# Optimization experiments

Measured on AMD Instinct MI355X. Metric: run time of the kernel, lower is better.

## Reference

```python
import jax, jax.numpy as jnp
import numpy as np

D_MODEL = 1024
N_HEADS = 16
HEAD_DIM = 64
BATCH = 4
SEQ = 2048


def setup_inputs() -> dict:
    key = jax.random.key(0)
    ks = jax.random.split(key, 5)
    scale = 1.0 / np.sqrt(D_MODEL)
    return {
        "x": jax.random.normal(ks[0], (BATCH, SEQ, D_MODEL), dtype=jnp.float32),
        "Wq": jax.random.normal(ks[1], (D_MODEL, N_HEADS * HEAD_DIM), dtype=jnp.float32) * scale,
        "Wk": jax.random.normal(ks[2], (D_MODEL, N_HEADS * HEAD_DIM), dtype=jnp.float32) * scale,
        "Wv": jax.random.normal(ks[3], (D_MODEL, N_HEADS * HEAD_DIM), dtype=jnp.float32) * scale,
        "Wo": jax.random.normal(ks[4], (N_HEADS * HEAD_DIM, D_MODEL), dtype=jnp.float32) * scale,
        "bo": jnp.zeros((D_MODEL,), dtype=jnp.float32),
    }


def reference(x, Wq, Wk, Wv, Wo, bo):
    B, S, _ = x.shape
    H, Dh = N_HEADS, HEAD_DIM
    # projections -> [B, H, S, Dh]
    q = (x @ Wq).reshape(B, S, H, Dh).transpose(0, 2, 1, 3)
    k = (x @ Wk).reshape(B, S, H, Dh).transpose(0, 2, 1, 3)
    v = (x @ Wv).reshape(B, S, H, Dh).transpose(0, 2, 1, 3)
    score = jnp.einsum("bhsd,bhtd->bhst", q, k) / jnp.sqrt(jnp.float32(Dh))
    causal = jnp.triu(jnp.ones((S, S), dtype=bool), k=1)
    score = jnp.where(causal, -jnp.inf, score)
    attn_probs = jax.nn.softmax(score, axis=-1)
    # dropout is identity in eval mode
    attn = jnp.einsum("bhst,bhtd->bhsd", attn_probs, v)
    out = attn.transpose(0, 2, 1, 3).reshape(B, S, H * Dh)
    out = out @ Wo + bo
    return (out, attn_probs)
```

## Files before the change

kernel.cpp:

```cpp
#include <hip/hip_runtime.h>
#include <hip/hip_bf16.h>

typedef __attribute__((ext_vector_type(8))) short bf16x8;
typedef __attribute__((ext_vector_type(4))) float f32x4;
typedef unsigned short ushort_t;
typedef unsigned int uint_t;

#define AS1 __attribute__((address_space(1)))
#define AS3 __attribute__((address_space(3)))

__constant__ int P4tab[16] = {0, 5, 10, 15, 1, 4, 11, 14, 2, 7, 8, 13, 3, 6, 9, 12};

__device__ __forceinline__ void gload_lds16(const void* g, void* l) {
    __builtin_amdgcn_global_load_lds((const AS1 void*)g, (AS3 void*)l, 16, 0, 0);
}

__device__ __forceinline__ ushort_t f2b(float f) {
    unsigned u = __builtin_bit_cast(unsigned, f);
    unsigned r = (u + 0x7FFFu + ((u >> 16) & 1u)) >> 16;
    return (ushort_t)r;
}

__global__ __launch_bounds__(256) void convert_x_kernel(const float* __restrict__ in,
                                                        ushort_t* __restrict__ out, int n4) {
    int i = blockIdx.x * blockDim.x + threadIdx.x;
    if (i < n4) {
        float4 f = ((const float4*)in)[i];
        ushort4 u;
        u.x = f2b(f.x); u.y = f2b(f.y); u.z = f2b(f.z); u.w = f2b(f.w);
        ((ushort4*)out)[i] = u;
    }
}

__global__ __launch_bounds__(256) void transpose_w_kernel(const float* __restrict__ W,
                                                          ushort_t* __restrict__ WT) {
    __shared__ float t[32][33];
    int n0 = blockIdx.x * 32, k0 = blockIdx.y * 32;
    int tx = threadIdx.x, ty = threadIdx.y;
    for (int i = 0; i < 4; ++i)
        t[ty + i * 8][tx] = W[(size_t)(k0 + ty + i * 8) * 1024 + n0 + tx];
    __syncthreads();
    for (int i = 0; i < 4; ++i)
        WT[(size_t)(n0 + ty + i * 8) * 1024 + k0 + tx] = f2b(t[tx][ty + i * 8]);
}

template <int N, int OUT_BF16>
__global__ __launch_bounds__(256) void gemm_kernel(const ushort_t* __restrict__ A,
                                                   const ushort_t* __restrict__ BT,
                                                   ushort_t* __restrict__ Cb,
                                                   float* __restrict__ Cf,
                                                   const float* __restrict__ bias) {
    const int K = 1024;
    __shared__ ushort_t As[3 * 128 * 32];
    __shared__ ushort_t Bs[3 * 128 * 32];
    int tid = threadIdx.x;
    int wid = tid >> 6, lane = tid & 63;
    int g = lane >> 4, lr = lane & 15;

    int zz = (int)blockIdx.x + 64 * (int)blockIdx.y;
    int nwg = 64 * (int)gridDim.y;
    int zs = (zz & 7) * (nwg >> 3) + (zz >> 3);
    int m0 = (zs % 64) * 128, n0 = (zs / 64) * 128;

    int wm = wid >> 1, wn = wid & 1;

    f32x4 acc[4][4] = {};

    int c0 = wid * 2;
    int lrow = lane >> 2;
    int lcol = ((lane & 3) ^ ((lane >> 3) & 3)) * 8;
    const ushort_t* Ag0 = A  + (size_t)(m0 + c0 * 16 + lrow) * K + lcol;
    const ushort_t* Ag1 = A  + (size_t)(m0 + c0 * 16 + 16 + lrow) * K + lcol;
    const ushort_t* Bg0 = BT + (size_t)(n0 + c0 * 16 + lrow) * K + lcol;
    const ushort_t* Bg1 = BT + (size_t)(n0 + c0 * 16 + 16 + lrow) * K + lcol;

    int swzA = ((lr >> 1) & 3) << 4;

    auto stage = [&](int si, int kt) {
        char* a0 = (char*)As + si * 8192 + c0 * 1024;
        char* b0 = (char*)Bs + si * 8192 + c0 * 1024;
        gload_lds16(Ag0 + kt * 32, a0);
        gload_lds16(Ag1 + kt * 32, a0 + 1024);
        gload_lds16(Bg0 + kt * 32, b0);
        gload_lds16(Bg1 + kt * 32, b0 + 1024);
    };

    stage(0, 0);
    stage(1, 1);
    asm volatile("s_waitcnt vmcnt(4)" ::: "memory");
    __builtin_amdgcn_s_barrier();
    __builtin_amdgcn_sched_barrier(0);
    for (int kt = 0; kt < 32; ++kt) {
        int nt = kt + 2;
        stage(nt % 3, nt < 32 ? nt : 31);
        const char* ab = (const char*)As + (kt % 3) * 8192;
        const char* bb = (const char*)Bs + (kt % 3) * 8192;
        bf16x8 af[4], bfr[4];
#pragma unroll
        for (int m = 0; m < 4; ++m) {
            int row = wm * 64 + m * 16 + lr;
            af[m] = *(const bf16x8*)(ab + row * 64 + ((g * 16) ^ swzA));
        }
#pragma unroll
        for (int n = 0; n < 4; ++n) {
            int row = wn * 64 + n * 16 + lr;
            bfr[n] = *(const bf16x8*)(bb + row * 64 + ((g * 16) ^ swzA));
        }
#pragma unroll
        for (int m = 0; m < 4; ++m)
#pragma unroll
            for (int n = 0; n < 4; ++n)
                acc[m][n] = __builtin_amdgcn_mfma_f32_16x16x32_bf16(af[m], bfr[n], acc[m][n], 0, 0, 0);
        asm volatile("s_waitcnt vmcnt(4)" ::: "memory");
        __builtin_amdgcn_s_barrier();
        __builtin_amdgcn_sched_barrier(0);
    }

#pragma unroll
    for (int m = 0; m < 4; ++m)
#pragma unroll
        for (int n = 0; n < 4; ++n) {
            int row0 = m0 + wm * 64 + m * 16 + g * 4;
            int col  = n0 + wn * 64 + n * 16 + lr;
#pragma unroll
            for (int r = 0; r < 4; ++r) {
                float v = acc[m][n][r];
                if (OUT_BF16)
                    Cb[(size_t)(row0 + r) * N + col] = f2b(v);
                else
                    Cf[(size_t)(row0 + r) * N + col] = v + bias[col];
            }
        }
}

__global__ __launch_bounds__(256) void vt_kernel(const ushort_t* __restrict__ Cqkv,
                                                 ushort_t* __restrict__ Vt) {
    int b = blockIdx.z, h = blockIdx.y, st = blockIdx.x;
    __shared__ ushort_t t[64][72];
    const ushort_t* src = Cqkv + (size_t)b * 2048 * 3072 + 2048 + (size_t)h * 64;
    int tid = threadIdx.x;
#pragma unroll
    for (int i = 0; i < 2; ++i) {
        int c = tid + i * 256;
        int sl = c >> 3, dc = (c & 7) * 8;
        *(bf16x8*)&t[sl][dc] = *(const bf16x8*)(src + (size_t)(st * 64 + sl) * 3072 + dc);
    }
    __syncthreads();
#pragma unroll
    for (int i = 0; i < 2; ++i) {
        int c = tid + i * 256;
        int d = c >> 3, sc = (c & 7) * 8;
        bf16x8 v;
#pragma unroll
        for (int j = 0; j < 8; ++j) v[j] = (short)t[sc + j][d];
        *(bf16x8*)(Vt + ((size_t)(b * 16 + h) * 64 + d) * 2048 + st * 64 + sc) = v;
    }
}

__global__ __launch_bounds__(256, 4) void attn_kernel(const ushort_t* __restrict__ Cqkv,
                                                      const ushort_t* __restrict__ Vtg,
                                                      float* __restrict__ Pout,
                                                      ushort_t* __restrict__ Oout) {
    const int S = 2048, DQ = 3072;
    const float C1 = 0.18033688f;
    const float C2 = 5.77078016f;

    int z = (int)blockIdx.x;
    int c = z & 255, j = z >> 8;
    int p = P4tab[(c & 3) * 4 + j];
    int h = (c >> 2) & 15, b = c >> 6;
    int qtA = p, qtB = 31 - p;

    int tid = threadIdx.x, wid = tid >> 6, lane = tid & 63;
    int g = lane >> 4, lr = lane & 15;
    int vsr = tid >> 2, vsc = (tid & 3) * 16;

    __shared__ ushort_t KV[4][4096];
    __shared__ ushort_t Pl[4096];
    char* PlB = (char*)Pl + wid * 2048;

    const ushort_t* Qb = Cqkv + (size_t)b * S * DQ + (size_t)h * 64;
    const ushort_t* Kb = Cqkv + (size_t)b * S * DQ + 1024 + (size_t)h * 64;
    const ushort_t* Vb = Vtg + (size_t)((b * 16 + h) * 64) * 2048;
    float* PbaseA = Pout + (((size_t)(b * 16 + h)) * S + qtA * 64) * S;
    float* PbaseB = Pout + (((size_t)(b * 16 + h)) * S + qtB * 64) * S;

    int srow = lane >> 3;
    int scol = ((lane & 7) ^ srow) * 8;

    auto zfill = [&](int zi) {
        float* base; int tt;
        if (zi < 31 - qtA) { base = PbaseA; tt = qtA + 1 + zi; }
        else               { base = PbaseB; tt = qtB + 1 + (zi - (31 - qtA)); }
        float* dst = base + (size_t)vsr * S + tt * 64 + vsc;
        f32x4 zf = {0.f, 0.f, 0.f, 0.f};
#pragma unroll
        for (int jj = 0; jj < 4; ++jj) ((f32x4*)dst)[jj] = zf;
    };

    auto stageK = [&](int ri, int tt) {
        char* dst = (char*)&KV[ri][0] + wid * 1024;
        gload_lds16(Kb + (size_t)(tt * 64 + wid * 8 + srow) * DQ + scol, dst);
        gload_lds16(Kb + (size_t)(tt * 64 + 32 + wid * 8 + srow) * DQ + scol, dst + 4096);
    };
    auto stageV = [&](int ri, int tt) {
        char* dst = (char*)&KV[2 + ri][0] + wid * 1024;
        gload_lds16(Vb + (size_t)(wid * 8 + srow) * 2048 + tt * 64 + scol, dst);
        gload_lds16(Vb + (size_t)(32 + wid * 8 + srow) * 2048 + tt * 64 + scol, dst + 4096);
    };
    auto stageK2 = [&](int ss, int t0, int t1) {
        char* dst = (char*)&KV[ss * 2][0] + wid * 1024;
        gload_lds16(Kb + (size_t)(t0 * 64 + wid * 8 + srow) * DQ + scol, dst);
        gload_lds16(Kb + (size_t)(t0 * 64 + 32 + wid * 8 + srow) * DQ + scol, dst + 4096);
        gload_lds16(Kb + (size_t)(t1 * 64 + wid * 8 + srow) * DQ + scol, dst + 8192);
        gload_lds16(Kb + (size_t)(t1 * 64 + 32 + wid * 8 + srow) * DQ + scol, dst + 12288);
    };

    bf16x8 qfA[2], qfB[2];
    {
        const ushort_t* qa = Qb + (size_t)(qtA * 64 + wid * 16 + lr) * DQ + g * 8;
        qfA[0] = *(const bf16x8*)qa;
        qfA[1] = *(const bf16x8*)(qa + 32);
        const ushort_t* qb2 = Qb + (size_t)(qtB * 64 + wid * 16 + lr) * DQ + g * 8;
        qfB[0] = *(const bf16x8*)qb2;
        qfB[1] = *(const bf16x8*)(qb2 + 32);
    }
    int qloc = wid * 16 + lr;

    float psA = 0.f, psB = 0.f;

    auto p1_tile = [&](const char* ksb, int tt) {
#pragma unroll
        for (int nb = 0; nb < 4; ++nb) {
            int row = nb * 16 + lr;
            int x = (row & 7) << 4;
            bf16x8 k0 = *(const bf16x8*)(ksb + row * 128 + ((g * 16) ^ x));
            bf16x8 k1 = *(const bf16x8*)(ksb + row * 128 + ((64 + g * 16) ^ x));
            f32x4 sB = {};
            sB = __builtin_amdgcn_mfma_f32_16x16x32_bf16(k0, qfB[0], sB, 0, 0, 0);
            sB = __builtin_amdgcn_mfma_f32_16x16x32_bf16(k1, qfB[1], sB, 0, 0, 0);
            if (tt == qtB) {
#pragma unroll
                for (int r = 0; r < 4; ++r)
                    if (nb * 16 + g * 4 + r <= qloc) psB += exp2f(fmaf(sB[r], C1, -C2));
            } else {
#pragma unroll
                for (int r = 0; r < 4; ++r) psB += exp2f(fmaf(sB[r], C1, -C2));
            }
            if (tt <= qtA) {
                f32x4 sA = {};
                sA = __builtin_amdgcn_mfma_f32_16x16x32_bf16(k0, qfA[0], sA, 0, 0, 0);
                sA = __builtin_amdgcn_mfma_f32_16x16x32_bf16(k1, qfA[1], sA, 0, 0, 0);
                if (tt == qtA) {
#pragma unroll
                    for (int r = 0; r < 4; ++r)
                        if (nb * 16 + g * 4 + r <= qloc) psA += exp2f(fmaf(sA[r], C1, -C2));
                } else {
#pragma unroll
                    for (int r = 0; r < 4; ++r) psA += exp2f(fmaf(sA[r], C1, -C2));
                }
            }
        }
    };

    int nR = (qtB + 2) >> 1;
    stageK2(0, 0, 1);
    asm volatile("s_waitcnt vmcnt(0)" ::: "memory");
    __builtin_amdgcn_s_barrier();
    __builtin_amdgcn_sched_barrier(0);
    for (int ri = 0; ri < nR; ++ri) {
        zfill(ri);
        int t0n = 2 * ri + 2, t1n = 2 * ri + 3;
        if (t0n > qtB) t0n = qtB;
        if (t1n > qtB) t1n = qtB;
        stageK2((ri + 1) & 1, t0n, t1n);
        const char* ksb = (const char*)&KV[(ri & 1) * 2][0];
        __builtin_amdgcn_s_setprio(1);
        p1_tile(ksb, 2 * ri);
        if (2 * ri + 1 <= qtB) p1_tile(ksb + 8192, 2 * ri + 1);
        __builtin_amdgcn_s_setprio(0);
        asm volatile("s_waitcnt vmcnt(0)" ::: "memory");
        __builtin_amdgcn_s_barrier();
        __builtin_amdgcn_sched_barrier(0);
    }
    psA += __shfl_xor(psA, 16); psA += __shfl_xor(psA, 32);
    psB += __shfl_xor(psB, 16); psB += __shfl_xor(psB, 32);
    float lnA = __log2f(psA) + C2;
    float lnB = __log2f(psB) + C2;

    f32x4 OA[4] = {}, OB[4] = {};
    stageK(0, 0);
    stageV(0, 0);
    __syncthreads();
    int buf = 0;
    for (int tt = 0; tt <= qtB; ++tt) {
        {
            int z0 = nR + 2 * tt;
            if (z0 < 31) { zfill(z0); if (z0 + 1 < 31) zfill(z0 + 1); }
        }
        if (tt < qtB) { stageK(buf ^ 1, tt + 1); stageV(buf ^ 1, tt + 1); }
        const char* ksb = (const char*)&KV[buf][0];
        const char* vsb = (const char*)&KV[2 + buf][0];

        {
            f32x4 pv[4];
            __builtin_amdgcn_s_setprio(1);
#pragma unroll
            for (int nb = 0; nb < 4; ++nb) {
                int row = nb * 16 + lr;
                int x = (row & 7) << 4;
                f32x4 s = {};
                s = __builtin_amdgcn_mfma_f32_16x16x32_bf16(*(const bf16x8*)(ksb + row * 128 + ((g * 16) ^ x)), qfB[0], s, 0, 0, 0);
                s = __builtin_amdgcn_mfma_f32_16x16x32_bf16(*(const bf16x8*)(ksb + row * 128 + ((64 + g * 16) ^ x)), qfB[1], s, 0, 0, 0);
#pragma unroll
                for (int r = 0; r < 4; ++r) {
                    float v = exp2f(fmaf(s[r], C1, -lnB));
                    if (tt == qtB && (nb * 16 + g * 4 + r > qloc)) v = 0.f;
                    pv[nb][r] = v;
                }
            }
            __builtin_amdgcn_s_setprio(0);
#pragma unroll
            for (int nb = 0; nb < 4; ++nb)
                *(f32x4*)(PbaseB + (size_t)qloc * S + tt * 64 + nb * 16 + g * 4) = pv[nb];
#pragma unroll
            for (int nb = 0; nb < 4; ++nb) {
                uint_t w0, w1;
                asm("v_cvt_pk_bf16_f32 %0, %1, %2" : "=v"(w0) : "v"(pv[nb][0]), "v"(pv[nb][1]));
                asm("v_cvt_pk_bf16_f32 %0, %1, %2" : "=v"(w1) : "v"(pv[nb][2]), "v"(pv[nb][3]));
                uint2 w; w.x = w0; w.y = w1;
                *(uint2*)(PlB + ((lr * 128 + nb * 32 + g * 8) ^ ((lr & 7) << 4))) = w;
            }
            __builtin_amdgcn_wave_barrier();
            __builtin_amdgcn_s_setprio(1);
#pragma unroll
            for (int kc = 0; kc < 2; ++kc) {
                bf16x8 pf = *(const bf16x8*)(PlB + ((lr * 128 + kc * 64 + g * 16) ^ ((lr & 7) << 4)));
#pragma unroll
                for (int nb = 0; nb < 4; ++nb) {
                    int vrow = nb * 16 + lr;
                    bf16x8 vf = *(const bf16x8*)(vsb + vrow * 128 + ((kc * 64 + g * 16) ^ ((vrow & 7) << 4)));
                    OB[nb] = __builtin_amdgcn_mfma_f32_16x16x32_bf16(pf, vf, OB[nb], 0, 0, 0);
                }
            }
            __builtin_amdgcn_s_setprio(0);
            __builtin_amdgcn_wave_barrier();
        }

        if (tt <= qtA) {
            f32x4 pv[4];
            __builtin_amdgcn_s_setprio(1);
#pragma unroll
            for (int nb = 0; nb < 4; ++nb) {
                int row = nb * 16 + lr;
                int x = (row & 7) << 4;
                f32x4 s = {};
                s = __builtin_amdgcn_mfma_f32_16x16x32_bf16(*(const bf16x8*)(ksb + row * 128 + ((g * 16) ^ x)), qfA[0], s, 0, 0, 0);
                s = __builtin_amdgcn_mfma_f32_16x16x32_bf16(*(const bf16x8*)(ksb + row * 128 + ((64 + g * 16) ^ x)), qfA[1], s, 0, 0, 0);
#pragma unroll
                for (int r = 0; r < 4; ++r) {
                    float v = exp2f(fmaf(s[r], C1, -lnA));
                    if (tt == qtA && (nb * 16 + g * 4 + r > qloc)) v = 0.f;
                    pv[nb][r] = v;
                }
            }
            __builtin_amdgcn_s_setprio(0);
#pragma unroll
            for (int nb = 0; nb < 4; ++nb)
                *(f32x4*)(PbaseA + (size_t)qloc * S + tt * 64 + nb * 16 + g * 4) = pv[nb];
#pragma unroll
            for (int nb = 0; nb < 4; ++nb) {
                uint_t w0, w1;
                asm("v_cvt_pk_bf16_f32 %0, %1, %2" : "=v"(w0) : "v"(pv[nb][0]), "v"(pv[nb][1]));
                asm("v_cvt_pk_bf16_f32 %0, %1, %2" : "=v"(w1) : "v"(pv[nb][2]), "v"(pv[nb][3]));
                uint2 w; w.x = w0; w.y = w1;
                *(uint2*)(PlB + ((lr * 128 + nb * 32 + g * 8) ^ ((lr & 7) << 4))) = w;
            }
            __builtin_amdgcn_wave_barrier();
            __builtin_amdgcn_s_setprio(1);
#pragma unroll
            for (int kc = 0; kc < 2; ++kc) {
                bf16x8 pf = *(const bf16x8*)(PlB + ((lr * 128 + kc * 64 + g * 16) ^ ((lr & 7) << 4)));
#pragma unroll
                for (int nb = 0; nb < 4; ++nb) {
                    int vrow = nb * 16 + lr;
                    bf16x8 vf = *(const bf16x8*)(vsb + vrow * 128 + ((kc * 64 + g * 16) ^ ((vrow & 7) << 4)));
                    OA[nb] = __builtin_amdgcn_mfma_f32_16x16x32_bf16(pf, vf, OA[nb], 0, 0, 0);
                }
            }
            __builtin_amdgcn_s_setprio(0);
            __builtin_amdgcn_wave_barrier();
            asm volatile("s_waitcnt vmcnt(8)" ::: "memory");
        } else {
            asm volatile("s_waitcnt vmcnt(4)" ::: "memory");
        }
        __builtin_amdgcn_s_barrier();
        __builtin_amdgcn_sched_barrier(0);
        buf ^= 1;
    }

#pragma unroll
    for (int nb = 0; nb < 4; ++nb)
#pragma unroll
        for (int r = 0; r < 4; ++r) {
            int qA = qtA * 64 + wid * 16 + g * 4 + r;
            int qB = qtB * 64 + wid * 16 + g * 4 + r;
            Oout[((size_t)b * S + qA) * 1024 + h * 64 + nb * 16 + lr] = f2b(OA[nb][r]);
            Oout[((size_t)b * S + qB) * 1024 + h * 64 + nb * 16 + lr] = f2b(OB[nb][r]);
        }
}

extern "C" void kernel_launch(void* const* d_in, const int* in_sizes, int n_in,
                              void* d_out, int out_size, void* d_ws, size_t ws_size,
                              hipStream_t stream) {
    const float* x  = (const float*)d_in[0];
    const float* Wq = (const float*)d_in[1];
    const float* Wk = (const float*)d_in[2];
    const float* Wv = (const float*)d_in[3];
    const float* Wo = (const float*)d_in[4];
    const float* bo = (const float*)d_in[5];

    float* out  = (float*)d_out;
    float* Pout = out + (size_t)8388608;

    char* ws = (char*)d_ws;
    ushort_t* xb    = (ushort_t*)(ws);
    ushort_t* wqkv  = (ushort_t*)(ws + (16u << 20));
    ushort_t* wob   = (ushort_t*)(ws + (22u << 20));
    ushort_t* Cqkv  = (ushort_t*)(ws + (24u << 20));
    ushort_t* Vtw   = (ushort_t*)(ws + (72u << 20));
    ushort_t* attnb = (ushort_t*)(ws + (104u << 20));

    convert_x_kernel<<<8192, 256, 0, stream>>>(x, xb, 2097152);
    transpose_w_kernel<<<dim3(32, 32), dim3(32, 8), 0, stream>>>(Wq, wqkv);
    transpose_w_kernel<<<dim3(32, 32), dim3(32, 8), 0, stream>>>(Wk, wqkv + 1024 * 1024);
    transpose_w_kernel<<<dim3(32, 32), dim3(32, 8), 0, stream>>>(Wv, wqkv + 2 * 1024 * 1024);
    transpose_w_kernel<<<dim3(32, 32), dim3(32, 8), 0, stream>>>(Wo, wob);

    gemm_kernel<3072, 1><<<dim3(64, 24), 256, 0, stream>>>(xb, wqkv, Cqkv, nullptr, nullptr);

    vt_kernel<<<dim3(32, 16, 4), 256, 0, stream>>>(Cqkv, Vtw);

    attn_kernel<<<1024, 256, 0, stream>>>(Cqkv, Vtw, Pout, attnb);

    gemm_kernel<1024, 0><<<dim3(64, 8), 256, 0, stream>>>(attnb, wob, nullptr, out, bo);
}
```

Measured before the change: 476.5 us.

## Split attention into row-sum pass and PV pass kernels, merge weight transposes

The fused attention kernel is split in two. The first kernel computes the softmax row log-sums with a lighter register and LDS footprint (launch bound raised to 5 blocks), and writes them to a workspace buffer. The second kernel reads those sums, recomputes the scores, and writes the probabilities and the PV output; all zero-filling of the masked region now happens in that second kernel. The four weight transpose launches are also merged into a single launch with a z dimension. The split adds a kernel launch and a small global round trip, and Q and K are read twice across two launches, in exchange for better occupancy in the sum pass.

```diff
diff --git a/kernel.cpp b/kernel.cpp
--- a/kernel.cpp
+++ b/kernel.cpp
@@ -32,9 +32,16 @@
     }
 }
 
-__global__ __launch_bounds__(256) void transpose_w_kernel(const float* __restrict__ W,
-                                                          ushort_t* __restrict__ WT) {
+__global__ __launch_bounds__(256) void transpose_w4_kernel(const float* __restrict__ W0,
+                                                           const float* __restrict__ W1,
+                                                           const float* __restrict__ W2,
+                                                           const float* __restrict__ W3,
+                                                           ushort_t* __restrict__ WTqkv,
+                                                           ushort_t* __restrict__ WTo) {
     __shared__ float t[32][33];
+    int which = blockIdx.z;
+    const float* W = (which == 0) ? W0 : (which == 1) ? W1 : (which == 2) ? W2 : W3;
+    ushort_t* WT = (which < 3) ? (WTqkv + (size_t)which * 1024 * 1024) : WTo;
     int n0 = blockIdx.x * 32, k0 = blockIdx.y * 32;
     int tx = threadIdx.x, ty = threadIdx.y;
     for (int i = 0; i < 4; ++i)
@@ -157,10 +164,8 @@
     }
 }
 
-__global__ __launch_bounds__(256, 4) void attn_kernel(const ushort_t* __restrict__ Cqkv,
-                                                      const ushort_t* __restrict__ Vtg,
-                                                      float* __restrict__ Pout,
-                                                      ushort_t* __restrict__ Oout) {
+__global__ __launch_bounds__(256, 5) void attn_sums_kernel(const ushort_t* __restrict__ Cqkv,
+                                                           float* __restrict__ lnlbuf) {
     const int S = 2048, DQ = 3072;
     const float C1 = 0.18033688f;
     const float C2 = 5.77078016f;
@@ -173,41 +178,15 @@
 
     int tid = threadIdx.x, wid = tid >> 6, lane = tid & 63;
     int g = lane >> 4, lr = lane & 15;
-    int vsr = tid >> 2, vsc = (tid & 3) * 16;
 
     __shared__ ushort_t KV[4][4096];
-    __shared__ ushort_t Pl[4096];
-    char* PlB = (char*)Pl + wid * 2048;
 
     const ushort_t* Qb = Cqkv + (size_t)b * S * DQ + (size_t)h * 64;
     const ushort_t* Kb = Cqkv + (size_t)b * S * DQ + 1024 + (size_t)h * 64;
-    const ushort_t* Vb = Vtg + (size_t)((b * 16 + h) * 64) * 2048;
-    float* PbaseA = Pout + (((size_t)(b * 16 + h)) * S + qtA * 64) * S;
-    float* PbaseB = Pout + (((size_t)(b * 16 + h)) * S + qtB * 64) * S;
 
     int srow = lane >> 3;
     int scol = ((lane & 7) ^ srow) * 8;
 
-    auto zfill = [&](int zi) {
-        float* base; int tt;
-        if (zi < 31 - qtA) { base = PbaseA; tt = qtA + 1 + zi; }
-        else               { base = PbaseB; tt = qtB + 1 + (zi - (31 - qtA)); }
-        float* dst = base + (size_t)vsr * S + tt * 64 + vsc;
-        f32x4 zf = {0.f, 0.f, 0.f, 0.f};
-#pragma unroll
-        for (int jj = 0; jj < 4; ++jj) ((f32x4*)dst)[jj] = zf;
-    };
-
-    auto stageK = [&](int ri, int tt) {
-        char* dst = (char*)&KV[ri][0] + wid * 1024;
-        gload_lds16(Kb + (size_t)(tt * 64 + wid * 8 + srow) * DQ + scol, dst);
-        gload_lds16(Kb + (size_t)(tt * 64 + 32 + wid * 8 + srow) * DQ + scol, dst + 4096);
-    };
-    auto stageV = [&](int ri, int tt) {
-        char* dst = (char*)&KV[2 + ri][0] + wid * 1024;
-        gload_lds16(Vb + (size_t)(wid * 8 + srow) * 2048 + tt * 64 + scol, dst);
-        gload_lds16(Vb + (size_t)(32 + wid * 8 + srow) * 2048 + tt * 64 + scol, dst + 4096);
-    };
     auto stageK2 = [&](int ss, int t0, int t1) {
         char* dst = (char*)&KV[ss * 2][0] + wid * 1024;
         gload_lds16(Kb + (size_t)(t0 * 64 + wid * 8 + srow) * DQ + scol, dst);
@@ -269,7 +248,6 @@
     __builtin_amdgcn_s_barrier();
     __builtin_amdgcn_sched_barrier(0);
     for (int ri = 0; ri < nR; ++ri) {
-        zfill(ri);
         int t0n = 2 * ri + 2, t1n = 2 * ri + 3;
         if (t0n > qtB) t0n = qtB;
         if (t1n > qtB) t1n = qtB;
@@ -285,8 +263,78 @@
     }
     psA += __shfl_xor(psA, 16); psA += __shfl_xor(psA, 32);
     psB += __shfl_xor(psB, 16); psB += __shfl_xor(psB, 32);
-    float lnA = __log2f(psA) + C2;
-    float lnB = __log2f(psB) + C2;
+    if (g == 0) {
+        float* dst = lnlbuf + (size_t)(b * 16 + h) * S;
+        dst[qtA * 64 + qloc] = __log2f(psA) + C2;
+        dst[qtB * 64 + qloc] = __log2f(psB) + C2;
+    }
+}
+
+__global__ __launch_bounds__(256, 4) void attn_pv_kernel(const ushort_t* __restrict__ Cqkv,
+                                                         const ushort_t* __restrict__ Vtg,
+                                                         const float* __restrict__ lnlbuf,
+                                                         float* __restrict__ Pout,
+                                                         ushort_t* __restrict__ Oout) {
+    const int S = 2048, DQ = 3072;
+    const float C1 = 0.18033688f;
+
+    int z = (int)blockIdx.x;
+    int c = z & 255, j = z >> 8;
+    int p = P4tab[(c & 3) * 4 + j];
+    int h = (c >> 2) & 15, b = c >> 6;
+    int qtA = p, qtB = 31 - p;
+
+    int tid = threadIdx.x, wid = tid >> 6, lane = tid & 63;
+    int g = lane >> 4, lr = lane & 15;
+    int vsr = tid >> 2, vsc = (tid & 3) * 16;
+
+    __shared__ ushort_t KV[4][4096];
+    __shared__ ushort_t Pl[4096];
+    char* PlB = (char*)Pl + wid * 2048;
+
+    const ushort_t* Qb = Cqkv + (size_t)b * S * DQ + (size_t)h * 64;
+    const ushort_t* Kb = Cqkv + (size_t)b * S * DQ + 1024 + (size_t)h * 64;
+    const ushort_t* Vb = Vtg + (size_t)((b * 16 + h) * 64) * 2048;
+    float* PbaseA = Pout + (((size_t)(b * 16 + h)) * S + qtA * 64) * S;
+    float* PbaseB = Pout + (((size_t)(b * 16 + h)) * S + qtB * 64) * S;
+
+    int srow = lane >> 3;
+    int scol = ((lane & 7) ^ srow) * 8;
+
+    auto zfill = [&](int zi) {
+        float* base; int tt;
+        if (zi < 31 - qtA) { base = PbaseA; tt = qtA + 1 + zi; }
+        else               { base = PbaseB; tt = qtB + 1 + (zi - (31 - qtA)); }
+        float* dst = base + (size_t)vsr * S + tt * 64 + vsc;
+        f32x4 zf = {0.f, 0.f, 0.f, 0.f};
+#pragma unroll
+        for (int jj = 0; jj < 4; ++jj) ((f32x4*)dst)[jj] = zf;
+    };
+
+    auto stageK = [&](int ri, int tt) {
+        char* dst = (char*)&KV[ri][0] + wid * 1024;
+        gload_lds16(Kb + (size_t)(tt * 64 + wid * 8 + srow) * DQ + scol, dst);
+        gload_lds16(Kb + (size_t)(tt * 64 + 32 + wid * 8 + srow) * DQ + scol, dst + 4096);
+    };
+    auto stageV = [&](int ri, int tt) {
+        char* dst = (char*)&KV[2 + ri][0] + wid * 1024;
+        gload_lds16(Vb + (size_t)(wid * 8 + srow) * 2048 + tt * 64 + scol, dst);
+        gload_lds16(Vb + (size_t)(32 + wid * 8 + srow) * 2048 + tt * 64 + scol, dst + 4096);
+    };
+
+    bf16x8 qfA[2], qfB[2];
+    {
+        const ushort_t* qa = Qb + (size_t)(qtA * 64 + wid * 16 + lr) * DQ + g * 8;
+        qfA[0] = *(const bf16x8*)qa;
+        qfA[1] = *(const bf16x8*)(qa + 32);
+        const ushort_t* qb2 = Qb + (size_t)(qtB * 64 + wid * 16 + lr) * DQ + g * 8;
+        qfB[0] = *(const bf16x8*)qb2;
+        qfB[1] = *(const bf16x8*)(qb2 + 32);
+    }
+    int qloc = wid * 16 + lr;
+
+    float lnA = lnlbuf[(size_t)(b * 16 + h) * S + qtA * 64 + qloc];
+    float lnB = lnlbuf[(size_t)(b * 16 + h) * S + qtB * 64 + qloc];
 
     f32x4 OA[4] = {}, OB[4] = {};
     stageK(0, 0);
@@ -295,7 +343,7 @@
     int buf = 0;
     for (int tt = 0; tt <= qtB; ++tt) {
         {
-            int z0 = nR + 2 * tt;
+            int z0 = 2 * tt;
             if (z0 < 31) { zfill(z0); if (z0 + 1 < 31) zfill(z0 + 1); }
         }
         if (tt < qtB) { stageK(buf ^ 1, tt + 1); stageV(buf ^ 1, tt + 1); }
@@ -430,18 +478,18 @@
     ushort_t* Cqkv  = (ushort_t*)(ws + (24u << 20));
     ushort_t* Vtw   = (ushort_t*)(ws + (72u << 20));
     ushort_t* attnb = (ushort_t*)(ws + (104u << 20));
+    float*    lnl   = (float*)(ws + (120u << 20));
 
     convert_x_kernel<<<8192, 256, 0, stream>>>(x, xb, 2097152);
-    transpose_w_kernel<<<dim3(32, 32), dim3(32, 8), 0, stream>>>(Wq, wqkv);
-    transpose_w_kernel<<<dim3(32, 32), dim3(32, 8), 0, stream>>>(Wk, wqkv + 1024 * 1024);
-    transpose_w_kernel<<<dim3(32, 32), dim3(32, 8), 0, stream>>>(Wv, wqkv + 2 * 1024 * 1024);
-    transpose_w_kernel<<<dim3(32, 32), dim3(32, 8), 0, stream>>>(Wo, wob);
+    transpose_w4_kernel<<<dim3(32, 32, 4), dim3(32, 8), 0, stream>>>(Wq, Wk, Wv, Wo, wqkv, wob);
 
     gemm_kernel<3072, 1><<<dim3(64, 24), 256, 0, stream>>>(xb, wqkv, Cqkv, nullptr, nullptr);
 
     vt_kernel<<<dim3(32, 16, 4), 256, 0, stream>>>(Cqkv, Vtw);
 
-    attn_kernel<<<1024, 256, 0, stream>>>(Cqkv, Vtw, Pout, attnb);
+    attn_sums_kernel<<<1024, 256, 0, stream>>>(Cqkv, lnl);
+
+    attn_pv_kernel<<<1024, 256, 0, stream>>>(Cqkv, Vtw, lnl, Pout, attnb);
 
     gemm_kernel<1024, 0><<<dim3(64, 8), 256, 0, stream>>>(attnb, wob, nullptr, out, bo);
 }
```

New measurement: 491.8 us. +3.2%, slower.
